# Performance work log

Hardware: AMD Instinct MI355X
Metric: run time of the kernel (lower is better)

The kernel has to match this reference:

```python
import jax, jax.numpy as jnp
import numpy as np


def _hard_sigmoid(x):
    # torch: clamp(0.2 * x + 0.5, 0, 1)
    return jnp.clip(0.2 * x + 0.5, 0.0, 1.0)


def _hardtanh(x):
    return jnp.clip(x, -1.0, 1.0)


def _run_dir(x, h0, c0, w_ih, w_hh, b):
    """One direction of a HardLSTM layer.
    x: [T, B, I], h0/c0: [B, H], w_ih: [4H, I], w_hh: [4H, H], b: [4H]
    (b is bias_ih + bias_hh of the original cell; identical math).
    """
    # Hoist the input projection out of the recurrence (one big GEMM).
    gx = jnp.einsum('tbi,gi->tbg', x, w_ih) + b  # [T, B, 4H]

    def step(carry, gx_t):
        h, c = carry
        gates = gx_t + h @ w_hh.T  # [B, 4H]
        i, f, g, o = jnp.split(gates, 4, axis=-1)
        i = _hard_sigmoid(i)
        f = _hard_sigmoid(f)
        g = _hardtanh(g)
        o = _hard_sigmoid(o)
        cy = f * c + i * g
        hy = o * _hardtanh(cy)
        return (hy, cy), hy

    (h, c), ys = jax.lax.scan(step, (h0, c0), gx)
    return ys, h, c


def _bidir_layer(x, h0, c0, w_ih, w_hh, b):
    """h0/c0: [2, B, H]; w_ih: [2, 4H, I]; w_hh: [2, 4H, H]; b: [2, 4H]."""
    yf, hf, cf = _run_dir(x, h0[0], c0[0], w_ih[0], w_hh[0], b[0])
    yb, hb, cb = _run_dir(x[::-1], h0[1], c0[1], w_ih[1], w_hh[1], b[1])
    yb = yb[::-1]
    # torch cat([yf.unsqueeze(2), yb.unsqueeze(2)], 2).view(T, B, 2H)
    y = jnp.concatenate([yf, yb], axis=-1)  # [T, B, 2H]
    return y, jnp.stack([hf, hb]), jnp.stack([cf, cb])


def reference(x, h0, c0, w_ih0, w_hh0, b0, w_ih1, w_hh1, b1):
    # Stacked 2-layer bidirectional HardLSTM, time-major input.
    y0, h_l0, c_l0 = _bidir_layer(x, h0[0:2], c0[0:2], w_ih0, w_hh0, b0)
    y1, h_l1, c_l1 = _bidir_layer(y0, h0[2:4], c0[2:4], w_ih1, w_hh1, b1)
    hn = jnp.concatenate([h_l0, h_l1], axis=0)  # [4, B, H]
    cn = jnp.concatenate([c_l0, c_l1], axis=0)
    return y1, hn, cn


def setup_inputs() -> dict:
    key = jax.random.key(0)
    ks = jax.random.split(key, 8)
    T, B, I, H = 512, 32, 512, 1024
    stdv = 1.0 / np.sqrt(H)  # matches reset_parameters uniform(-stdv, stdv) scale
    FGB = 1.0  # forget_gate_bias

    x = jax.random.normal(ks[0], (T, B, I), dtype=jnp.float32)
    h0 = jnp.zeros((4, B, H), dtype=jnp.float32)
    c0 = jnp.zeros((4, B, H), dtype=jnp.float32)

    def mk_w(k, shape):
        return (jax.random.normal(k, shape, dtype=jnp.float32) * stdv).astype(jnp.float32)

    w_ih0 = mk_w(ks[1], (2, 4 * H, I))
    w_hh0 = mk_w(ks[2], (2, 4 * H, H))
    b0 = mk_w(ks[3], (2, 4 * H))
    w_ih1 = mk_w(ks[4], (2, 4 * H, 2 * H))
    w_hh1 = mk_w(ks[5], (2, 4 * H, H))
    b1 = mk_w(ks[6], (2, 4 * H))
    # forget gate bias override (bias_ih forget slice = FGB, bias_hh = 0 -> sum = FGB)
    b0 = b0.at[:, H:2 * H].set(FGB)
    b1 = b1.at[:, H:2 * H].set(FGB)

    return {"x": x, "h0": h0, "c0": c0,
            "w_ih0": w_ih0, "w_hh0": w_hh0, "b0": b0,
            "w_ih1": w_ih1, "w_hh1": w_hh1, "b1": b1}
```

## Files before the change

### kernel.cpp

```cpp
#include <hip/hip_runtime.h>
#include <cstdint>


typedef _Float16 half8 __attribute__((ext_vector_type(8)));
typedef _Float16 half4v __attribute__((ext_vector_type(4)));
typedef float floatx4 __attribute__((ext_vector_type(4)));
typedef int int4v __attribute__((ext_vector_type(4)));

#define T_LEN 512
#define BATCH 32
#define HID 1024
#define NTB 16384
#define UPW 32
#define WPD 32

__device__ __forceinline__ float hsig(float x) {
  return fminf(fmaxf(fmaf(0.2f, x, 0.5f), 0.0f), 1.0f);
}
__device__ __forceinline__ float htanh(float x) {
  return fminf(fmaxf(x, -1.0f), 1.0f);
}

__device__ __forceinline__ int4v load_co16(const void* p) {
  int4v r;
  asm volatile("global_load_dwordx4 %0, %1, off sc0 sc1"
               : "=&v"(r) : "v"(p) : "memory");
  return r;
}
__device__ __forceinline__ void store_co4(void* p, int v) {
  asm volatile("global_store_dword %0, %1, off sc0 sc1"
               :: "v"(p), "v"(v) : "memory");
}
__device__ __forceinline__ void waitcnt0() {
  asm volatile("s_waitcnt vmcnt(0)" ::: "memory");
}
__device__ __forceinline__ void barrier_lgkm() {
  asm volatile("s_waitcnt lgkmcnt(0)" ::: "memory");
  __builtin_amdgcn_sched_barrier(0);
  __builtin_amdgcn_s_barrier();
  __builtin_amdgcn_sched_barrier(0);
}

__device__ __forceinline__ void gll16(const void* g, void* l) {
  __builtin_amdgcn_global_load_lds((const __attribute__((address_space(1))) void*)g,
                                   (__attribute__((address_space(3))) void*)l,
                                   16, 0, 0);
}

__device__ __forceinline__ void gate_xpose(floatx4 v, bool i1, bool i0,
                                           float& gI, float& gF,
                                           float& gG, float& gO) {
  float s0 = i1 ? v[0] : v[2], s1 = i1 ? v[1] : v[3];
  float r0 = __shfl_xor(s0, 32), r1 = __shfl_xor(s1, 32);
  float A0 = i1 ? r0 : v[0], A1 = i1 ? r1 : v[1];
  float A2 = i1 ? v[2] : r0, A3 = i1 ? v[3] : r1;
  s0 = i0 ? A0 : A1; s1 = i0 ? A2 : A3;
  r0 = __shfl_xor(s0, 16); r1 = __shfl_xor(s1, 16);
  gI = i0 ? r0 : A0; gF = i0 ? A1 : r0;
  gG = i0 ? r1 : A2; gO = i0 ? A3 : r1;
}

__device__ __forceinline__ int pack_u8_fk(int q, int fk) {
  int p = __shfl_xor(q, 16);
  int d = (fk & 1) ? ((p & 0xff) | ((q & 0xff) << 8))
                   : ((q & 0xff) | ((p & 0xff) << 8));
  int d2 = __shfl_xor(d, 32);
  return (d & 0xffff) | (d2 << 16);
}

__global__ __launch_bounds__(256) void cvt_f32_f16(const float* __restrict__ s,
                                                   _Float16* __restrict__ d,
                                                   int n4) {
  int i = blockIdx.x * blockDim.x + threadIdx.x;
  int stride = gridDim.x * blockDim.x;
  for (; i < n4; i += stride) {
    float4 v = ((const float4*)s)[i];
    half4v h = {(_Float16)v.x, (_Float16)v.y, (_Float16)v.z, (_Float16)v.w};
    ((half4v*)d)[i] = h;
  }
}

__global__ __launch_bounds__(256) void gemm_gx(const _Float16* __restrict__ A,
                                               const _Float16* __restrict__ B,
                                               const float* __restrict__ bias,
                                               _Float16* __restrict__ C,
                                               int K) {
  __shared__ __align__(16) _Float16 A_s[128 * 64];
  __shared__ __align__(16) _Float16 B_s[128 * 64];
  const int tid = threadIdx.x;
  const int lane = tid & 63;
  const int w = tid >> 6;
  const int bm = blockIdx.x >> 7;
  const int bn = blockIdx.x & 127;
  const int m0 = bm * 128, n0 = bn * 128;

  floatx4 acc[4][4] = {};

  const int srow = w * 8 + (lane >> 3);
  const int scol = ((lane & 7) ^ ((lane >> 3) & 7)) * 8;
  const _Float16* Ag = A + (size_t)(m0 + srow) * K + scol;
  const _Float16* Bg = B + (size_t)(n0 + srow) * K + scol;
  char* As_base = (char*)A_s + (size_t)(w * 8) * 128;
  char* Bs_base = (char*)B_s + (size_t)(w * 8) * 128;

  const int wm = (w >> 1) * 64;
  const int wn = (w & 1) * 64;
  const int fr = lane & 15;
  const int fk = lane >> 4;

  for (int kb = 0; kb < K; kb += 64) {
#pragma unroll
    for (int i = 0; i < 4; ++i) {
      gll16(Ag + (size_t)i * 32 * K + kb, As_base + i * 32 * 128);
      gll16(Bg + (size_t)i * 32 * K + kb, Bs_base + i * 32 * 128);
    }
    __syncthreads();
#pragma unroll
    for (int kt = 0; kt < 2; ++kt) {
      half8 af[4], bf[4];
#pragma unroll
      for (int mi = 0; mi < 4; ++mi) {
        int row = wm + mi * 16 + fr;
        int k8 = kt * 4 + fk;
        af[mi] = *(const half8*)(A_s + row * 64 + ((k8 ^ (row & 7)) << 3));
      }
#pragma unroll
      for (int ni = 0; ni < 4; ++ni) {
        int row = wn + ni * 16 + fr;
        int k8 = kt * 4 + fk;
        bf[ni] = *(const half8*)(B_s + row * 64 + ((k8 ^ (row & 7)) << 3));
      }
#pragma unroll
      for (int mi = 0; mi < 4; ++mi)
#pragma unroll
        for (int ni = 0; ni < 4; ++ni)
          acc[mi][ni] = __builtin_amdgcn_mfma_f32_16x16x32_f16(af[mi], bf[ni],
                                                               acc[mi][ni], 0, 0, 0);
    }
    __syncthreads();
  }

#pragma unroll
  for (int mi = 0; mi < 4; ++mi) {
    int rowb = m0 + wm + mi * 16 + fk * 4;
#pragma unroll
    for (int r = 0; r < 4; ++r) {
      float bv = bias[rowb + r];
#pragma unroll
      for (int ni = 0; ni < 4; ++ni) {
        int col = n0 + wn + ni * 16 + fr;
        C[(size_t)(rowb + r) * NTB + col] = (_Float16)(acc[mi][ni][r] + bv);
      }
    }
  }
}

__global__
__attribute__((amdgpu_flat_work_group_size(512, 512), amdgpu_waves_per_eu(2, 2)))
void recur(const _Float16* __restrict__ gx,
           const _Float16* __restrict__ whh,
           const float* __restrict__ h0,
           const float* __restrict__ c0,
           unsigned char* __restrict__ hbuf,
           int* __restrict__ flags,
           int layer,
           _Float16* __restrict__ yf16,
           float* __restrict__ yf32,
           float* __restrict__ hn,
           float* __restrict__ cn) {
  __shared__ __align__(16) _Float16 h_s[BATCH * HID];

  const int tid = threadIdx.x;
  const int lane = tid & 63;
  const int w = tid >> 6;
  const int dir = blockIdx.x >> 5;
  const int wgd = blockIdx.x & 31;
  const int u0 = wgd * UPW;
  const int fr = lane & 15, fk = lane >> 4;

  half8 af[32];
  float rowsum = 0.f;
  {
    const int g = fr >> 2, du = fr & 3;
    const _Float16* wrow = whh + ((size_t)dir * 4096 + g * 1024 + u0 + w * 4 + du) * HID;
#pragma unroll
    for (int kt = 0; kt < 32; ++kt) {
      half8 raw = *(const half8*)(wrow + kt * 32 + fk * 8);
      half8 s;
#pragma unroll
      for (int e2 = 0; e2 < 8; ++e2) {
        float v = (float)raw[e2] * (1.f / 127.f);
        s[e2] = (_Float16)v;
        rowsum += (float)s[e2];
      }
      af[kt] = s;
    }
  }
#pragma unroll
  for (int kt = 0; kt < 32; ++kt)
    asm volatile("" : "+v"(af[kt]));

  rowsum += __shfl_xor(rowsum, 16);
  rowsum += __shfl_xor(rowsum, 32);
  float corr0 = 1152.f * __shfl(rowsum, fk * 4 + 0);
  float corr1 = 1152.f * __shfl(rowsum, fk * 4 + 1);
  float corr2 = 1152.f * __shfl(rowsum, fk * 4 + 2);
  float corr3 = 1152.f * __shfl(rowsum, fk * 4 + 3);

  const int unit = u0 + w * 4 + fk;
  const int batA = fr, batB = 16 + fr;
  const size_t st0 = (size_t)(layer * 2 + dir) * (BATCH * HID);
  float cA = c0[st0 + (size_t)batA * HID + unit];
  float cB = c0[st0 + (size_t)batB * HID + unit];

  unsigned char* buf0 = hbuf + (size_t)dir * 32768;
  unsigned char* buf1 = hbuf + (size_t)(2 + dir) * 32768;
  int* fl = flags + dir * WPD;

  {
    float hA0 = h0[st0 + (size_t)batA * HID + unit];
    float hB0 = h0[st0 + (size_t)batB * HID + unit];
    int qA = (int)rintf(fminf(fmaxf(hA0, -1.f), 1.f) * 127.f) + 128;
    int qB = (int)rintf(fminf(fmaxf(hB0, -1.f), 1.f) * 127.f) + 128;
    int dwA = pack_u8_fk(qA, fk);
    int dwB = pack_u8_fk(qB, fk);
    if (fk == 0) {
      store_co4(buf0 + (size_t)batA * HID + u0 + w * 4, dwA);
      store_co4(buf0 + (size_t)batB * HID + u0 + w * 4, dwB);
    }
    waitcnt0();
    barrier_lgkm();
    if (tid == 0) store_co4(fl + wgd, 1);
  }

  const size_t GS = (size_t)1024 * NTB;
  const _Float16* gxp = gx + ((size_t)dir * 4096 + unit) * NTB;

  int ts0 = dir ? (T_LEN - 1) : 0;
  float gxiA = (float)gxp[0 * GS + (size_t)ts0 * BATCH + batA];
  float gxfA = (float)gxp[1 * GS + (size_t)ts0 * BATCH + batA];
  float gxgA = (float)gxp[2 * GS + (size_t)ts0 * BATCH + batA];
  float gxoA = (float)gxp[3 * GS + (size_t)ts0 * BATCH + batA];
  float gxiB = (float)gxp[0 * GS + (size_t)ts0 * BATCH + batB];
  float gxfB = (float)gxp[1 * GS + (size_t)ts0 * BATCH + batB];
  float gxgB = (float)gxp[2 * GS + (size_t)ts0 * BATCH + batB];
  float gxoB = (float)gxp[3 * GS + (size_t)ts0 * BATCH + batB];

  const bool i1 = (fk >> 1) & 1, i0 = fk & 1;
  const unsigned c64 = 0x64646464u;
  const int e = (tid + wgd * 8) & 511;
  const int eb = e >> 6, el = e & 63;

  for (int t = 0; t < T_LEN; ++t) {
    if (w == 0) {
      const int want = t + 1;
      for (;;) {
        int v;
        asm volatile("global_load_dword %0, %1, off sc0 sc1\n\ts_waitcnt vmcnt(0)"
                     : "=&v"(v) : "v"(fl + (lane & 31)) : "memory");
        if (__all(v >= want)) break;
        __builtin_amdgcn_s_sleep(2);
      }
    }
    barrier_lgkm();

    const unsigned char* src = (t & 1) ? buf1 : buf0;
    unsigned char* dst = (t & 1) ? buf0 : buf1;

    int4v u8v[4];
#pragma unroll
    for (int cc = 0; cc < 4; ++cc)
      u8v[cc] = load_co16(src + cc * 8192 + e * 16);
    waitcnt0();
#pragma unroll
    for (int cc = 0; cc < 4; ++cc) {
      int b = cc * 8 + eb;
      int lslot = el * 2;
      char* row = (char*)h_s + b * 2048;
      int swz = (b & 7) << 4;
      int4v A, B2;
      A[0]  = __builtin_amdgcn_perm(c64, (unsigned)u8v[cc][0], 0x05010400u);
      A[1]  = __builtin_amdgcn_perm(c64, (unsigned)u8v[cc][0], 0x07030602u);
      A[2]  = __builtin_amdgcn_perm(c64, (unsigned)u8v[cc][1], 0x05010400u);
      A[3]  = __builtin_amdgcn_perm(c64, (unsigned)u8v[cc][1], 0x07030602u);
      B2[0] = __builtin_amdgcn_perm(c64, (unsigned)u8v[cc][2], 0x05010400u);
      B2[1] = __builtin_amdgcn_perm(c64, (unsigned)u8v[cc][2], 0x07030602u);
      B2[2] = __builtin_amdgcn_perm(c64, (unsigned)u8v[cc][3], 0x05010400u);
      B2[3] = __builtin_amdgcn_perm(c64, (unsigned)u8v[cc][3], 0x07030602u);
      *(int4v*)(row + ((lslot * 16) ^ swz)) = A;
      *(int4v*)(row + (((lslot + 1) * 16) ^ swz)) = B2;
    }

    int tn = (t + 1 < T_LEN) ? t + 1 : t;
    int tsn = dir ? (T_LEN - 1 - tn) : tn;
    float ngxiA = (float)gxp[0 * GS + (size_t)tsn * BATCH + batA];
    float ngxfA = (float)gxp[1 * GS + (size_t)tsn * BATCH + batA];
    float ngxgA = (float)gxp[2 * GS + (size_t)tsn * BATCH + batA];
    float ngxoA = (float)gxp[3 * GS + (size_t)tsn * BATCH + batA];
    float ngxiB = (float)gxp[0 * GS + (size_t)tsn * BATCH + batB];
    float ngxfB = (float)gxp[1 * GS + (size_t)tsn * BATCH + batB];
    float ngxgB = (float)gxp[2 * GS + (size_t)tsn * BATCH + batB];
    float ngxoB = (float)gxp[3 * GS + (size_t)tsn * BATCH + batB];

    barrier_lgkm();

    floatx4 aA0 = {-corr0, -corr1, -corr2, -corr3};
    floatx4 aB0 = {-corr0, -corr1, -corr2, -corr3};
    floatx4 aA1 = {0.f, 0.f, 0.f, 0.f}, aB1 = {0.f, 0.f, 0.f, 0.f};
    {
      const char* hpA = (const char*)h_s + batA * 2048;
      const char* hpB = (const char*)h_s + batB * 2048;
      const int bxA = (batA & 7) << 4;
      const int bxB = (batB & 7) << 4;
#pragma unroll
      for (int kt = 0; kt < 32; kt += 2) {
        half8 b0A = *(const half8*)(hpA + ((kt * 64 + fk * 16) ^ bxA));
        half8 b0B = *(const half8*)(hpB + ((kt * 64 + fk * 16) ^ bxB));
        half8 b1A = *(const half8*)(hpA + (((kt + 1) * 64 + fk * 16) ^ bxA));
        half8 b1B = *(const half8*)(hpB + (((kt + 1) * 64 + fk * 16) ^ bxB));
        aA0 = __builtin_amdgcn_mfma_f32_16x16x32_f16(af[kt], b0A, aA0, 0, 0, 0);
        aB0 = __builtin_amdgcn_mfma_f32_16x16x32_f16(af[kt], b0B, aB0, 0, 0, 0);
        aA1 = __builtin_amdgcn_mfma_f32_16x16x32_f16(af[kt + 1], b1A, aA1, 0, 0, 0);
        aB1 = __builtin_amdgcn_mfma_f32_16x16x32_f16(af[kt + 1], b1B, aB1, 0, 0, 0);
      }
    }
    floatx4 vA = aA0 + aA1, vB = aB0 + aB1;

    float gI, gF, gG, gO;
    gate_xpose(vA, i1, i0, gI, gF, gG, gO);
    float igA = hsig(gI + gxiA);
    float fgA = hsig(gF + gxfA);
    float ggA = htanh(gG + gxgA);
    float ogA = hsig(gO + gxoA);
    cA = fgA * cA + igA * ggA;
    float hA = ogA * htanh(cA);

    gate_xpose(vB, i1, i0, gI, gF, gG, gO);
    float igB = hsig(gI + gxiB);
    float fgB = hsig(gF + gxfB);
    float ggB = htanh(gG + gxgB);
    float ogB = hsig(gO + gxoB);
    cB = fgB * cB + igB * ggB;
    float hB = ogB * htanh(cB);

    gxiA = ngxiA; gxfA = ngxfA; gxgA = ngxgA; gxoA = ngxoA;
    gxiB = ngxiB; gxfB = ngxfB; gxgB = ngxgB; gxoB = ngxoB;

    const int tseq = dir ? (T_LEN - 1 - t) : t;

    if (t == T_LEN - 1) {
      size_t oA = st0 + (size_t)batA * HID + unit;
      size_t oB = st0 + (size_t)batB * HID + unit;
      hn[oA] = hA; cn[oA] = cA;
      hn[oB] = hB; cn[oB] = cB;
    } else {
      int qA = (int)rintf(hA * 127.f) + 128;
      int qB = (int)rintf(hB * 127.f) + 128;
      int dwA = pack_u8_fk(qA, fk);
      int dwB = pack_u8_fk(qB, fk);
      if (fk == 0) {
        store_co4(dst + (size_t)batA * HID + u0 + w * 4, dwA);
        store_co4(dst + (size_t)batB * HID + u0 + w * 4, dwB);
      }
      waitcnt0();
      barrier_lgkm();
      if (tid == 0) store_co4(fl + wgd, t + 2);
    }

    size_t yA = ((size_t)tseq * BATCH + batA) * 2048 + (size_t)dir * 1024 + unit;
    size_t yB = ((size_t)tseq * BATCH + batB) * 2048 + (size_t)dir * 1024 + unit;
    if (yf16) { yf16[yA] = (_Float16)hA; yf16[yB] = (_Float16)hB; }
    else      { yf32[yA] = hA;           yf32[yB] = hB; }
  }
}

extern "C" void kernel_launch(void* const* d_in, const int* in_sizes, int n_in,
                              void* d_out, int out_size, void* d_ws, size_t ws_size,
                              hipStream_t stream) {
  const float* x    = (const float*)d_in[0];
  const float* h0   = (const float*)d_in[1];
  const float* c0   = (const float*)d_in[2];
  const float* wih0 = (const float*)d_in[3];
  const float* whh0 = (const float*)d_in[4];
  const float* b0   = (const float*)d_in[5];
  const float* wih1 = (const float*)d_in[6];
  const float* whh1 = (const float*)d_in[7];
  const float* b1   = (const float*)d_in[8];
  float* out = (float*)d_out;

  char* ws = (char*)d_ws;
  size_t off = 0;
  int* flags = (int*)ws;                          off += 4096;
  unsigned char* hbuf = (unsigned char*)(ws + off); off += 262144;
  _Float16* xh    = (_Float16*)(ws + off);    off += (size_t)8388608 * 2;
  _Float16* wih0h = (_Float16*)(ws + off);    off += (size_t)4194304 * 2;
  _Float16* whh0h = (_Float16*)(ws + off);    off += (size_t)8388608 * 2;
  _Float16* wih1h = (_Float16*)(ws + off);    off += (size_t)16777216 * 2;
  _Float16* whh1h = (_Float16*)(ws + off);    off += (size_t)8388608 * 2;
  _Float16* y0h   = (_Float16*)(ws + off);    off += (size_t)33554432 * 2;
  _Float16* gxbuf = (_Float16*)(ws + off);    off += (size_t)134217728 * 2;

  hipMemsetAsync(flags, 0, 4096, stream);

  cvt_f32_f16<<<2048, 256, 0, stream>>>(x,    xh,    8388608 / 4);
  cvt_f32_f16<<<2048, 256, 0, stream>>>(wih0, wih0h, 4194304 / 4);
  cvt_f32_f16<<<2048, 256, 0, stream>>>(whh0, whh0h, 8388608 / 4);
  cvt_f32_f16<<<2048, 256, 0, stream>>>(wih1, wih1h, 16777216 / 4);
  cvt_f32_f16<<<2048, 256, 0, stream>>>(whh1, whh1h, 8388608 / 4);

  float* hn = out + 33554432;
  float* cn = out + 33685504;

  gemm_gx<<<8192, 256, 0, stream>>>(wih0h, xh, b0, gxbuf, 512);
  recur<<<64, 512, 0, stream>>>(gxbuf, whh0h, h0, c0, hbuf, flags, 0,
                                y0h, nullptr, hn, cn);
  gemm_gx<<<8192, 256, 0, stream>>>(wih1h, y0h, b1, gxbuf, 2048);
  recur<<<64, 512, 0, stream>>>(gxbuf, whh1h, h0, c0, hbuf + 131072, flags + 128, 1,
                                nullptr, out, hn, cn);
}
```

Baseline: 5.768 ms.

## Replace flag-based inter-block sync with zero-sentinel data polling on quad buffers

Drops the per-workgroup flag counters and the wave-0 spin on them. Each step's quantized h values (offset so they are never zero) now act as their own readiness signal: readers poll the source buffer until no byte is zero. A ring of four buffers is used, and the buffer two steps ahead is cleared back to zero. This removes a flag write, a waitcnt/barrier pair and a flag-poll round trip per timestep, at the cost of busy-polling on data and extra zeroing stores. Correctness depends on the store ordering across blocks behaving as the sentinel scheme assumes.

```diff
diff --git a/kernel.cpp b/kernel.cpp
--- a/kernel.cpp
+++ b/kernel.cpp
@@ -45,6 +45,10 @@
   __builtin_amdgcn_global_load_lds((const __attribute__((address_space(1))) void*)g,
                                    (__attribute__((address_space(3))) void*)l,
                                    16, 0, 0);
+}
+
+__device__ __forceinline__ unsigned haszero(unsigned v) {
+  return (v - 0x01010101u) & ~v & 0x80808080u;
 }
 
 __device__ __forceinline__ void gate_xpose(floatx4 v, bool i1, bool i0,
@@ -162,7 +166,6 @@
            const float* __restrict__ h0,
            const float* __restrict__ c0,
            unsigned char* __restrict__ hbuf,
-           int* __restrict__ flags,
            int layer,
            _Float16* __restrict__ yf16,
            float* __restrict__ yf32,
@@ -213,9 +216,10 @@
   float cA = c0[st0 + (size_t)batA * HID + unit];
   float cB = c0[st0 + (size_t)batB * HID + unit];
 
-  unsigned char* buf0 = hbuf + (size_t)dir * 32768;
-  unsigned char* buf1 = hbuf + (size_t)(2 + dir) * 32768;
-  int* fl = flags + dir * WPD;
+  unsigned char* bufs[4];
+#pragma unroll
+  for (int k = 0; k < 4; ++k)
+    bufs[k] = hbuf + ((size_t)dir * 4 + k) * 32768;
 
   {
     float hA0 = h0[st0 + (size_t)batA * HID + unit];
@@ -225,12 +229,9 @@
     int dwA = pack_u8_fk(qA, fk);
     int dwB = pack_u8_fk(qB, fk);
     if (fk == 0) {
-      store_co4(buf0 + (size_t)batA * HID + u0 + w * 4, dwA);
-      store_co4(buf0 + (size_t)batB * HID + u0 + w * 4, dwB);
-    }
-    waitcnt0();
-    barrier_lgkm();
-    if (tid == 0) store_co4(fl + wgd, 1);
+      store_co4(bufs[0] + (size_t)batA * HID + u0 + w * 4, dwA);
+      store_co4(bufs[0] + (size_t)batB * HID + u0 + w * 4, dwB);
+    }
   }
 
   const size_t GS = (size_t)1024 * NTB;
@@ -252,26 +253,31 @@
   const int eb = e >> 6, el = e & 63;
 
   for (int t = 0; t < T_LEN; ++t) {
-    if (w == 0) {
-      const int want = t + 1;
-      for (;;) {
-        int v;
-        asm volatile("global_load_dword %0, %1, off sc0 sc1\n\ts_waitcnt vmcnt(0)"
-                     : "=&v"(v) : "v"(fl + (lane & 31)) : "memory");
-        if (__all(v >= want)) break;
-        __builtin_amdgcn_s_sleep(2);
-      }
-    }
-    barrier_lgkm();
-
-    const unsigned char* src = (t & 1) ? buf1 : buf0;
-    unsigned char* dst = (t & 1) ? buf0 : buf1;
+    const unsigned char* src = bufs[t & 3];
+    unsigned char* dst  = bufs[(t + 1) & 3];
+    unsigned char* zdst = bufs[(t + 2) & 3];
 
     int4v u8v[4];
 #pragma unroll
     for (int cc = 0; cc < 4; ++cc)
       u8v[cc] = load_co16(src + cc * 8192 + e * 16);
     waitcnt0();
+    for (;;) {
+      unsigned bad = 0;
+#pragma unroll
+      for (int cc = 0; cc < 4; ++cc) {
+        unsigned z = haszero((unsigned)u8v[cc][0]) | haszero((unsigned)u8v[cc][1])
+                   | haszero((unsigned)u8v[cc][2]) | haszero((unsigned)u8v[cc][3]);
+        bad |= (z ? 1u : 0u) << cc;
+      }
+      if (bad == 0) break;
+#pragma unroll
+      for (int cc = 0; cc < 4; ++cc)
+        if (bad & (1u << cc))
+          u8v[cc] = load_co16(src + cc * 8192 + e * 16);
+      waitcnt0();
+    }
+
 #pragma unroll
     for (int cc = 0; cc < 4; ++cc) {
       int b = cc * 8 + eb;
@@ -361,16 +367,17 @@
       if (fk == 0) {
         store_co4(dst + (size_t)batA * HID + u0 + w * 4, dwA);
         store_co4(dst + (size_t)batB * HID + u0 + w * 4, dwB);
-      }
-      waitcnt0();
-      barrier_lgkm();
-      if (tid == 0) store_co4(fl + wgd, t + 2);
+        store_co4(zdst + (size_t)batA * HID + u0 + w * 4, 0);
+        store_co4(zdst + (size_t)batB * HID + u0 + w * 4, 0);
+      }
     }
 
     size_t yA = ((size_t)tseq * BATCH + batA) * 2048 + (size_t)dir * 1024 + unit;
     size_t yB = ((size_t)tseq * BATCH + batB) * 2048 + (size_t)dir * 1024 + unit;
     if (yf16) { yf16[yA] = (_Float16)hA; yf16[yB] = (_Float16)hB; }
     else      { yf32[yA] = hA;           yf32[yB] = hB; }
+
+    barrier_lgkm();
   }
 }
 
@@ -390,8 +397,7 @@
 
   char* ws = (char*)d_ws;
   size_t off = 0;
-  int* flags = (int*)ws;                          off += 4096;
-  unsigned char* hbuf = (unsigned char*)(ws + off); off += 262144;
+  unsigned char* hbuf = (unsigned char*)ws;   off += 524288;
   _Float16* xh    = (_Float16*)(ws + off);    off += (size_t)8388608 * 2;
   _Float16* wih0h = (_Float16*)(ws + off);    off += (size_t)4194304 * 2;
   _Float16* whh0h = (_Float16*)(ws + off);    off += (size_t)8388608 * 2;
@@ -400,7 +406,7 @@
   _Float16* y0h   = (_Float16*)(ws + off);    off += (size_t)33554432 * 2;
   _Float16* gxbuf = (_Float16*)(ws + off);    off += (size_t)134217728 * 2;
 
-  hipMemsetAsync(flags, 0, 4096, stream);
+  hipMemsetAsync(hbuf, 0, 524288, stream);
 
   cvt_f32_f16<<<2048, 256, 0, stream>>>(x,    xh,    8388608 / 4);
   cvt_f32_f16<<<2048, 256, 0, stream>>>(wih0, wih0h, 4194304 / 4);
@@ -412,9 +418,9 @@
   float* cn = out + 33685504;
 
   gemm_gx<<<8192, 256, 0, stream>>>(wih0h, xh, b0, gxbuf, 512);
-  recur<<<64, 512, 0, stream>>>(gxbuf, whh0h, h0, c0, hbuf, flags, 0,
+  recur<<<64, 512, 0, stream>>>(gxbuf, whh0h, h0, c0, hbuf, 0,
                                 y0h, nullptr, hn, cn);
   gemm_gx<<<8192, 256, 0, stream>>>(wih1h, y0h, b1, gxbuf, 2048);
-  recur<<<64, 512, 0, stream>>>(gxbuf, whh1h, h0, c0, hbuf + 131072, flags + 128, 1,
+  recur<<<64, 512, 0, stream>>>(gxbuf, whh1h, h0, c0, hbuf + 262144, 1,
                                 nullptr, out, hn, cn);
 }
```

New measurement: 6.632 ms. 1.15x slower.
